# Kernel tuning notes

Measured on AMD Instinct MI355X. Metric: run time of the kernel, lower is better.

Reference implementation:

```python
import jax, jax.numpy as jnp
import numpy as np

B, C, P, HP, WP = 128, 3, 196, 16, 16  # batch, channels, patches, patch h, patch w
E = 768  # embedding size; patches_pixel_count = C*HP*WP = 768


def setup_inputs() -> dict:
    key = jax.random.key(0)
    ks = jax.random.split(key, 9)
    return {
        "inputs": jax.random.normal(ks[0], (B, C, P, HP, WP), dtype=jnp.float32),
        "W1": jax.random.normal(ks[1], (C * HP * WP, 32), dtype=jnp.float32) * 0.02,
        "b1": jax.random.normal(ks[2], (32,), dtype=jnp.float32) * 0.02,
        "W2": jax.random.normal(ks[3], (32, 64), dtype=jnp.float32) * 0.02,
        "b2": jax.random.normal(ks[4], (64,), dtype=jnp.float32) * 0.02,
        "W3": jax.random.normal(ks[5], (64, E), dtype=jnp.float32) * 0.02,
        "b3": jax.random.normal(ks[6], (E,), dtype=jnp.float32) * 0.02,
        "cls_token": jax.random.normal(ks[7], (1, E), dtype=jnp.float32) * 0.02,
        "pos_enc": jax.random.normal(ks[8], (P + 1, E), dtype=jnp.float32) * 0.02,
    }


def reference(inputs, W1, b1, W2, b2, W3, b3, cls_token, pos_enc):
    b, c, p, hp, wp = inputs.shape
    # per-patch slab is [C, hp, wp] flattened in (C, h, w) order -> [B, P, C*hp*wp]
    x = jnp.transpose(inputs, (0, 2, 1, 3, 4)).reshape(b, p, c * hp * wp)
    x = x @ W1 + b1          # [B, P, 32]
    x = x @ W2 + b2          # [B, P, 64]
    x = x @ W3 + b3          # [B, P, E]
    cls = jnp.broadcast_to(cls_token[None], (b, 1, cls_token.shape[-1]))
    x = jnp.concatenate([cls, x], axis=1)  # [B, P+1, E]
    return x + pos_enc[None]               # broadcast add of position encodings
```

## Files before the change

kernel.cpp:

```cpp
#include <hip/hip_runtime.h>


#define BATCH 128
#define CH    3
#define NP    196
#define PIX   256
#define K1    768
#define NH    64
#define EMB   768
#define NROW  (BATCH * NP)

typedef __bf16 bf16x8 __attribute__((ext_vector_type(8)));
typedef float  f32x4  __attribute__((ext_vector_type(4)));

#define W12T_OFF 0
#define W3T_OFF  98304
#define B12_OFF  196608
#define POSB_OFF 196864
#define H_OFF    802048

__global__ __launch_bounds__(256) void patchembed_prep1(
    const float* __restrict__ W1, const float* __restrict__ W2,
    const float* __restrict__ b1, const float* __restrict__ b2,
    __bf16* __restrict__ w12t, float* __restrict__ b12)
{
    const int i = blockIdx.x * 256 + threadIdx.x;
    if (i < NH * K1) {
        const int n = i / K1, k = i - n * K1;
        float s = 0.f;
        #pragma unroll
        for (int j = 0; j < 32; ++j) s += W1[k * 32 + j] * W2[j * NH + n];
        w12t[i] = (__bf16)s;
    } else if (i < NH * K1 + NH) {
        const int n = i - NH * K1;
        float s = b2[n];
        #pragma unroll
        for (int j = 0; j < 32; ++j) s += b1[j] * W2[j * NH + n];
        b12[n] = s;
    }
}

__global__ __launch_bounds__(256) void patchembed_prep2(
    const float* __restrict__ W3, const float* __restrict__ b3,
    const float* __restrict__ cls, const float* __restrict__ pos,
    const float* __restrict__ b12,
    __bf16* __restrict__ w3t, float* __restrict__ posb, float* __restrict__ out)
{
    const int i = blockIdx.x * 256 + threadIdx.x;
    const int T1 = EMB * NH;
    const int T2 = T1 + 197 * EMB;
    const int T3 = T2 + BATCH * EMB;
    if (i < T1) {
        const int col = i >> 6, kk = i & 63;
        w3t[i] = (__bf16)W3[kk * EMB + col];
    } else if (i < T2) {
        const int j = i - T1;
        const int r = j / EMB, c = j - r * EMB;
        float v = pos[j];
        if (r == 0) {
            v += cls[c];
        } else {
            float s = b3[c];
            #pragma unroll
            for (int n = 0; n < NH; ++n) s += b12[n] * W3[n * EMB + c];
            v += s;
        }
        posb[j] = v;
    } else if (i < T3) {
        const int j = i - T2;
        const int b = j / EMB, c = j - b * EMB;
        out[b * (197 * EMB) + c] = cls[c] + pos[c];
    }
}

__global__ __launch_bounds__(256) void patchembed_s1(
    const float* __restrict__ X,
    const __bf16* __restrict__ w12t,
    __bf16* __restrict__ H)
{
    __shared__ __align__(16) float h1p[4][16][68];

    const int tid  = threadIdx.x;
    const int wv   = tid >> 6;
    const int lane = tid & 63;
    const int l15  = lane & 15;
    const int q    = lane >> 4;
    const int r0   = blockIdx.x * 16;

    {
        const int xrow = r0 + l15;
        const int b = xrow / NP, p = xrow - b * NP;
        const float* xb = X + ((b * CH) * NP + p) * PIX;
        const int kb0 = wv * 6;

        f32x4 acc0 = {0.f, 0.f, 0.f, 0.f};
        f32x4 acc1 = acc0, acc2 = acc0, acc3 = acc0;
        #pragma unroll
        for (int t = 0; t < 6; ++t) {
            const int kb = kb0 + t;
            const float* ptr = xb + (kb >> 3) * (NP * PIX) + (kb & 7) * 32 + q * 8;
            float4 u = *(const float4*)ptr;
            float4 v = *(const float4*)(ptr + 4);
            bf16x8 a;
            a[0] = (__bf16)u.x; a[1] = (__bf16)u.y;
            a[2] = (__bf16)u.z; a[3] = (__bf16)u.w;
            a[4] = (__bf16)v.x; a[5] = (__bf16)v.y;
            a[6] = (__bf16)v.z; a[7] = (__bf16)v.w;
            const __bf16* wb = w12t + kb * 32 + q * 8;
            bf16x8 f0 = *(const bf16x8*)(wb + l15 * K1);
            bf16x8 f1 = *(const bf16x8*)(wb + (16 + l15) * K1);
            bf16x8 f2 = *(const bf16x8*)(wb + (32 + l15) * K1);
            bf16x8 f3 = *(const bf16x8*)(wb + (48 + l15) * K1);
            acc0 = __builtin_amdgcn_mfma_f32_16x16x32_bf16(a, f0, acc0, 0, 0, 0);
            acc1 = __builtin_amdgcn_mfma_f32_16x16x32_bf16(a, f1, acc1, 0, 0, 0);
            acc2 = __builtin_amdgcn_mfma_f32_16x16x32_bf16(a, f2, acc2, 0, 0, 0);
            acc3 = __builtin_amdgcn_mfma_f32_16x16x32_bf16(a, f3, acc3, 0, 0, 0);
        }
        #pragma unroll
        for (int r = 0; r < 4; ++r) {
            h1p[wv][q * 4 + r][l15]      = acc0[r];
            h1p[wv][q * 4 + r][16 + l15] = acc1[r];
            h1p[wv][q * 4 + r][32 + l15] = acc2[r];
            h1p[wv][q * 4 + r][48 + l15] = acc3[r];
        }
    }
    __syncthreads();

    if (wv == 0) {
        f32x4 s0a = {0.f, 0.f, 0.f, 0.f};
        f32x4 s0b = s0a, s1a = s0a, s1b = s0a;
        #pragma unroll
        for (int w = 0; w < 4; ++w) {
            const float* hp = &h1p[w][l15][0];
            s0a += *(const f32x4*)(hp + q * 8);
            s0b += *(const f32x4*)(hp + q * 8 + 4);
            s1a += *(const f32x4*)(hp + 32 + q * 8);
            s1b += *(const f32x4*)(hp + 32 + q * 8 + 4);
        }
        bf16x8 a0, a1;
        #pragma unroll
        for (int j = 0; j < 4; ++j) {
            a0[j] = (__bf16)s0a[j]; a0[4 + j] = (__bf16)s0b[j];
            a1[j] = (__bf16)s1a[j]; a1[4 + j] = (__bf16)s1b[j];
        }
        __bf16* hr = H + (r0 + l15) * NH;
        *(bf16x8*)(hr + q * 8)      = a0;
        *(bf16x8*)(hr + 32 + q * 8) = a1;
    }
}

__global__ __launch_bounds__(256) void patchembed_s2(
    const __bf16* __restrict__ H,
    const __bf16* __restrict__ w3t,
    const float*  __restrict__ posb,
    float* __restrict__ out)
{
    const int tid  = threadIdx.x;
    const int wv   = tid >> 6;
    const int lane = tid & 63;
    const int l15  = lane & 15;
    const int q    = lane >> 4;

    const int wave_id = blockIdx.x * 4 + wv;
    const int rt = wave_id >> 3;
    const int cs = wave_id & 7;
    const int r0 = rt * 16;

    const __bf16* hr = H + (r0 + l15) * NH;
    bf16x8 a0 = *(const bf16x8*)(hr + q * 8);
    bf16x8 a1 = *(const bf16x8*)(hr + 32 + q * 8);

    int obase[4], pbase[4];
    #pragma unroll
    for (int r = 0; r < 4; ++r) {
        const int row = r0 + q * 4 + r;
        const int b = row / NP, p = row - b * NP;
        obase[r] = (b * 197 + p + 1) * EMB;
        pbase[r] = (p + 1) * EMB;
    }

    const int c0 = cs * 96 + l15;
    #pragma unroll
    for (int t = 0; t < 6; ++t) {
        const int col = c0 + t * 16;
        const __bf16* wr = w3t + col * NH;
        bf16x8 f0 = *(const bf16x8*)(wr + q * 8);
        bf16x8 f1 = *(const bf16x8*)(wr + 32 + q * 8);
        float pb0 = posb[pbase[0] + col];
        float pb1 = posb[pbase[1] + col];
        float pb2 = posb[pbase[2] + col];
        float pb3 = posb[pbase[3] + col];
        f32x4 z = {0.f, 0.f, 0.f, 0.f};
        f32x4 c = __builtin_amdgcn_mfma_f32_16x16x32_bf16(a0, f0, z, 0, 0, 0);
        c       = __builtin_amdgcn_mfma_f32_16x16x32_bf16(a1, f1, c, 0, 0, 0);
        out[obase[0] + col] = c[0] + pb0;
        out[obase[1] + col] = c[1] + pb1;
        out[obase[2] + col] = c[2] + pb2;
        out[obase[3] + col] = c[3] + pb3;
    }
}

extern "C" void kernel_launch(void* const* d_in, const int* in_sizes, int n_in,
                              void* d_out, int out_size, void* d_ws, size_t ws_size,
                              hipStream_t stream)
{
    const float* X   = (const float*)d_in[0];
    const float* W1  = (const float*)d_in[1];
    const float* b1  = (const float*)d_in[2];
    const float* W2  = (const float*)d_in[3];
    const float* b2  = (const float*)d_in[4];
    const float* W3  = (const float*)d_in[5];
    const float* b3  = (const float*)d_in[6];
    const float* cls = (const float*)d_in[7];
    const float* pos = (const float*)d_in[8];
    float* out = (float*)d_out;

    char* ws = (char*)d_ws;
    __bf16* w12t = (__bf16*)(ws + W12T_OFF);
    __bf16* w3t  = (__bf16*)(ws + W3T_OFF);
    float*  b12  = (float*)(ws + B12_OFF);
    float*  posb = (float*)(ws + POSB_OFF);
    __bf16* H    = (__bf16*)(ws + H_OFF);

    patchembed_prep1<<<193, 256, 0, stream>>>(W1, W2, b1, b2, w12t, b12);
    patchembed_prep2<<<1167, 256, 0, stream>>>(W3, b3, cls, pos, b12, w3t, posb, out);
    patchembed_s1<<<NROW / 16, 256, 0, stream>>>(X, w12t, H);
    patchembed_s2<<<NROW / 16 * 2, 256, 0, stream>>>(H, w3t, posb, out);
}
```

Before: 189.5 us.

## Merge prep kernels, swap MFMA operands for vectorized output stores, split H reduction

Result: slower. 212.3 us (+12.0%).

```diff
diff --git a/kernel.cpp b/kernel.cpp
--- a/kernel.cpp
+++ b/kernel.cpp
@@ -11,62 +11,48 @@
 #define NROW  (BATCH * NP)
 
 typedef __bf16 bf16x8 __attribute__((ext_vector_type(8)));
+typedef __bf16 bf16x4 __attribute__((ext_vector_type(4)));
 typedef float  f32x4  __attribute__((ext_vector_type(4)));
 
 #define W12T_OFF 0
 #define W3T_OFF  98304
-#define B12_OFF  196608
-#define POSB_OFF 196864
-#define H_OFF    802048
+#define BF_OFF   196608
+#define H_OFF    199680
 
-__global__ __launch_bounds__(256) void patchembed_prep1(
+__global__ __launch_bounds__(256) void patchembed_prep(
     const float* __restrict__ W1, const float* __restrict__ W2,
     const float* __restrict__ b1, const float* __restrict__ b2,
-    __bf16* __restrict__ w12t, float* __restrict__ b12)
+    const float* __restrict__ W3, const float* __restrict__ b3,
+    const float* __restrict__ cls, const float* __restrict__ pos,
+    __bf16* __restrict__ w12t, __bf16* __restrict__ w3t,
+    float* __restrict__ bf, float* __restrict__ out)
 {
     const int i = blockIdx.x * 256 + threadIdx.x;
-    if (i < NH * K1) {
+    const int T0 = NH * K1;
+    const int T1 = T0 + EMB;
+    const int T2 = T1 + EMB * NH;
+
+    if (i < T0) {
         const int n = i / K1, k = i - n * K1;
         float s = 0.f;
         #pragma unroll
         for (int j = 0; j < 32; ++j) s += W1[k * 32 + j] * W2[j * NH + n];
         w12t[i] = (__bf16)s;
-    } else if (i < NH * K1 + NH) {
-        const int n = i - NH * K1;
-        float s = b2[n];
-        #pragma unroll
-        for (int j = 0; j < 32; ++j) s += b1[j] * W2[j * NH + n];
-        b12[n] = s;
-    }
-}
-
-__global__ __launch_bounds__(256) void patchembed_prep2(
-    const float* __restrict__ W3, const float* __restrict__ b3,
-    const float* __restrict__ cls, const float* __restrict__ pos,
-    const float* __restrict__ b12,
-    __bf16* __restrict__ w3t, float* __restrict__ posb, float* __restrict__ out)
-{
-    const int i = blockIdx.x * 256 + threadIdx.x;
-    const int T1 = EMB * NH;
-    const int T2 = T1 + 197 * EMB;
-    const int T3 = T2 + BATCH * EMB;
-    if (i < T1) {
-        const int col = i >> 6, kk = i & 63;
-        w3t[i] = (__bf16)W3[kk * EMB + col];
+    } else if (i < T1) {
+        const int c = i - T0;
+        float s = b3[c];
+        for (int n = 0; n < NH; ++n) {
+            float t = b2[n];
+            #pragma unroll
+            for (int j = 0; j < 32; ++j) t += b1[j] * W2[j * NH + n];
+            s += t * W3[n * EMB + c];
+        }
+        bf[c] = s;
     } else if (i < T2) {
         const int j = i - T1;
-        const int r = j / EMB, c = j - r * EMB;
-        float v = pos[j];
-        if (r == 0) {
-            v += cls[c];
-        } else {
-            float s = b3[c];
-            #pragma unroll
-            for (int n = 0; n < NH; ++n) s += b12[n] * W3[n * EMB + c];
-            v += s;
-        }
-        posb[j] = v;
-    } else if (i < T3) {
+        const int col = j >> 6, kk = j & 63;
+        w3t[j] = (__bf16)W3[kk * EMB + col];
+    } else {
         const int j = i - T2;
         const int b = j / EMB, c = j - b * EMB;
         out[b * (197 * EMB) + c] = cls[c] + pos[c];
@@ -126,33 +112,24 @@
     }
     __syncthreads();
 
-    if (wv == 0) {
-        f32x4 s0a = {0.f, 0.f, 0.f, 0.f};
-        f32x4 s0b = s0a, s1a = s0a, s1b = s0a;
+    {
+        const int c0 = wv * 16 + q * 4;
+        f32x4 s = {0.f, 0.f, 0.f, 0.f};
         #pragma unroll
-        for (int w = 0; w < 4; ++w) {
-            const float* hp = &h1p[w][l15][0];
-            s0a += *(const f32x4*)(hp + q * 8);
-            s0b += *(const f32x4*)(hp + q * 8 + 4);
-            s1a += *(const f32x4*)(hp + 32 + q * 8);
-            s1b += *(const f32x4*)(hp + 32 + q * 8 + 4);
-        }
-        bf16x8 a0, a1;
+        for (int w = 0; w < 4; ++w)
+            s += *(const f32x4*)&h1p[w][l15][c0];
+        bf16x4 hv;
         #pragma unroll
-        for (int j = 0; j < 4; ++j) {
-            a0[j] = (__bf16)s0a[j]; a0[4 + j] = (__bf16)s0b[j];
-            a1[j] = (__bf16)s1a[j]; a1[4 + j] = (__bf16)s1b[j];
-        }
-        __bf16* hr = H + (r0 + l15) * NH;
-        *(bf16x8*)(hr + q * 8)      = a0;
-        *(bf16x8*)(hr + 32 + q * 8) = a1;
+        for (int j = 0; j < 4; ++j) hv[j] = (__bf16)s[j];
+        *(bf16x4*)(H + (r0 + l15) * NH + c0) = hv;
     }
 }
 
 __global__ __launch_bounds__(256) void patchembed_s2(
     const __bf16* __restrict__ H,
     const __bf16* __restrict__ w3t,
-    const float*  __restrict__ posb,
+    const float*  __restrict__ bf,
+    const float*  __restrict__ pos,
     float* __restrict__ out)
 {
     const int tid  = threadIdx.x;
@@ -167,36 +144,27 @@
     const int r0 = rt * 16;
 
     const __bf16* hr = H + (r0 + l15) * NH;
-    bf16x8 a0 = *(const bf16x8*)(hr + q * 8);
-    bf16x8 a1 = *(const bf16x8*)(hr + 32 + q * 8);
+    bf16x8 hb0 = *(const bf16x8*)(hr + q * 8);
+    bf16x8 hb1 = *(const bf16x8*)(hr + 32 + q * 8);
 
-    int obase[4], pbase[4];
-    #pragma unroll
-    for (int r = 0; r < 4; ++r) {
-        const int row = r0 + q * 4 + r;
-        const int b = row / NP, p = row - b * NP;
-        obase[r] = (b * 197 + p + 1) * EMB;
-        pbase[r] = (p + 1) * EMB;
-    }
+    const int row = r0 + l15;
+    const int b = row / NP, p = row - b * NP;
+    float* orow = out + (b * 197 + p + 1) * EMB;
+    const float* prow = pos + (p + 1) * EMB;
 
-    const int c0 = cs * 96 + l15;
     #pragma unroll
     for (int t = 0; t < 6; ++t) {
-        const int col = c0 + t * 16;
-        const __bf16* wr = w3t + col * NH;
-        bf16x8 f0 = *(const bf16x8*)(wr + q * 8);
-        bf16x8 f1 = *(const bf16x8*)(wr + 32 + q * 8);
-        float pb0 = posb[pbase[0] + col];
-        float pb1 = posb[pbase[1] + col];
-        float pb2 = posb[pbase[2] + col];
-        float pb3 = posb[pbase[3] + col];
+        const int colb = cs * 96 + t * 16;
+        const __bf16* wr = w3t + (colb + l15) * NH;
+        bf16x8 wa0 = *(const bf16x8*)(wr + q * 8);
+        bf16x8 wa1 = *(const bf16x8*)(wr + 32 + q * 8);
         f32x4 z = {0.f, 0.f, 0.f, 0.f};
-        f32x4 c = __builtin_amdgcn_mfma_f32_16x16x32_bf16(a0, f0, z, 0, 0, 0);
-        c       = __builtin_amdgcn_mfma_f32_16x16x32_bf16(a1, f1, c, 0, 0, 0);
-        out[obase[0] + col] = c[0] + pb0;
-        out[obase[1] + col] = c[1] + pb1;
-        out[obase[2] + col] = c[2] + pb2;
-        out[obase[3] + col] = c[3] + pb3;
+        f32x4 c = __builtin_amdgcn_mfma_f32_16x16x32_bf16(wa0, hb0, z, 0, 0, 0);
+        c       = __builtin_amdgcn_mfma_f32_16x16x32_bf16(wa1, hb1, c, 0, 0, 0);
+        const int c4 = colb + q * 4;
+        f32x4 pv = *(const f32x4*)(prow + c4);
+        f32x4 bv = *(const f32x4*)(bf + c4);
+        *(f32x4*)(orow + c4) = c + pv + bv;
     }
 }
 
@@ -218,12 +186,11 @@
     char* ws = (char*)d_ws;
     __bf16* w12t = (__bf16*)(ws + W12T_OFF);
     __bf16* w3t  = (__bf16*)(ws + W3T_OFF);
-    float*  b12  = (float*)(ws + B12_OFF);
-    float*  posb = (float*)(ws + POSB_OFF);
+    float*  bf   = (float*)(ws + BF_OFF);
     __bf16* H    = (__bf16*)(ws + H_OFF);
 
-    patchembed_prep1<<<193, 256, 0, stream>>>(W1, W2, b1, b2, w12t, b12);
-    patchembed_prep2<<<1167, 256, 0, stream>>>(W3, b3, cls, pos, b12, w3t, posb, out);
+    patchembed_prep<<<771, 256, 0, stream>>>(W1, W2, b1, b2, W3, b3, cls, pos,
+                                             w12t, w3t, bf, out);
     patchembed_s1<<<NROW / 16, 256, 0, stream>>>(X, w12t, H);
-    patchembed_s2<<<NROW / 16 * 2, 256, 0, stream>>>(H, w3t, posb, out);
+    patchembed_s2<<<NROW / 16 * 2, 256, 0, stream>>>(H, w3t, bf, pos, out);
 }
```
